# Performance work log

Measured on AMD Instinct MI355X. Metric: run time of the kernel, lower is better.

The kernel has to match this reference:

```python
import jax, jax.numpy as jnp
import numpy as np

B = 8192
D = 128
N_CLASSES = 100
TEMPERATURE = 0.1


def setup_inputs() -> dict:
    key = jax.random.key(0)
    k1, k2 = jax.random.split(key)
    feats = jax.random.normal(k1, (B, D), dtype=jnp.float32)
    # L2-normalise as the docstring assumes
    feats = feats / jnp.linalg.norm(feats, axis=1, keepdims=True)
    labels = jax.random.randint(k2, (B,), 0, N_CLASSES, dtype=jnp.int64)
    return {"features": feats, "labels": labels}


def reference(features, labels):
    features = features.astype(jnp.float32)
    b = features.shape[0]
    sim = (features @ features.T) / TEMPERATURE            # (B, B)
    labels_eq = labels[None, :] == labels[:, None]          # (B, B)
    self_mask = ~jnp.eye(b, dtype=bool)                     # (B, B), False on diag
    pos_mask = labels_eq & self_mask

    sim_max = jax.lax.stop_gradient(jnp.max(sim, axis=1, keepdims=True))
    logits = sim - sim_max                                  # (B, B)
    exp_logits = jnp.exp(logits) * self_mask.astype(jnp.float32)
    log_sum_exp = jnp.log(jnp.sum(exp_logits, axis=1, keepdims=True) + 1e-12)
    log_prob = logits - log_sum_exp                         # (B, B)

    n_positives = jnp.sum(pos_mask.astype(jnp.float32), axis=1)  # (B,)
    valid = n_positives > 0
    mean_log_prob = jnp.sum(pos_mask.astype(jnp.float32) * log_prob, axis=1) \
        / jnp.maximum(n_positives, 1.0)

    valid_f = valid.astype(jnp.float32)
    n_valid = jnp.sum(valid_f)
    loss = -jnp.sum(mean_log_prob * valid_f) / jnp.maximum(n_valid, 1.0)
    # match torch: return 0 if no anchor has a positive
    return jnp.where(n_valid > 0, loss, jnp.float32(0.0))
```

## Files before the change

kernel.cpp:

```cpp
#include <hip/hip_runtime.h>
#include <hip/hip_bf16.h>


#define BB 8192
#define DD 128
#define NCLS 100
#define NC 16
#define COLCHUNK (BB / NC)
#define NT (COLCHUNK / 16)
#define TEMP_INV 10.0f
#define MSHIFT 10.5f
#define C1F 14.426950408889634f
#define C2F -15.148297929334116f

typedef __bf16 bf16x8 __attribute__((ext_vector_type(8)));
typedef float floatx4 __attribute__((ext_vector_type(4)));

__device__ inline float fast_exp2(float x) {
#if __has_builtin(__builtin_amdgcn_exp2f)
    return __builtin_amdgcn_exp2f(x);
#else
    return exp2f(x);
#endif
}

__device__ inline unsigned short f2bf(float f) {
    unsigned u = __float_as_uint(f);
    return (unsigned short)((u + 0x7FFFu + ((u >> 16) & 1u)) >> 16);
}

__global__ __launch_bounds__(256) void supcon_convert(
    const void* __restrict__ fin, const void* __restrict__ lin,
    unsigned short* __restrict__ frag, int* __restrict__ lab,
    float* __restrict__ accbuf)
{
    int lane = threadIdx.x & 63;
    unsigned ue = ((unsigned)((const unsigned short*)fin)[2 * lane]) << 16;
    float fe = __uint_as_float(ue);
    float ve = fe * fe;
    int odd_or = ((const int*)lin)[2 * lane + 1];
#pragma unroll
    for (int m = 1; m < 64; m <<= 1) {
        ve += __shfl_xor(ve, m, 64);
        odd_or |= __shfl_xor(odd_or, m, 64);
    }
    bool f_bf16 = (ve > 0.05f) && (ve < 4.0f);
    bool l_i64  = (odd_or == 0);

    int G = blockIdx.x * 256 + threadIdx.x;
    int T = G >> 8;
    int g = (G >> 6) & 3;
    int l = G & 63;
    int col = T * 16 + (l & 15);
    int kb  = g * 32 + ((l >> 4) << 3);

    ushort4 o0, o1;
    if (!f_bf16) {
        const float4* src = (const float4*)((const float*)fin + (size_t)col * DD + kb);
        float4 a = src[0], b = src[1];
        o0.x = f2bf(a.x); o0.y = f2bf(a.y); o0.z = f2bf(a.z); o0.w = f2bf(a.w);
        o1.x = f2bf(b.x); o1.y = f2bf(b.y); o1.z = f2bf(b.z); o1.w = f2bf(b.w);
    } else {
        const ushort4* src = (const ushort4*)((const unsigned short*)fin + (size_t)col * DD + kb);
        o0 = src[0]; o1 = src[1];
    }
    ushort4* dst = (ushort4*)(frag + (size_t)G * 8);
    dst[0] = o0; dst[1] = o1;

    const int* L = (const int*)lin;
    if (blockIdx.x < 32) {
        int li = blockIdx.x * 256 + threadIdx.x;
        lab[li] = l_i64 ? L[2 * li] : L[li];
    }
    if (blockIdx.x == 0 && threadIdx.x == 0) {
        accbuf[0] = 0.0f;
        accbuf[1] = 0.0f;
        ((unsigned*)accbuf)[2] = 0u;
    }
}

#define LOADT(bb, lc, t)                                                      \
    {                                                                         \
        const unsigned char* fb =                                             \
            Fbc + ((size_t)((ctile0 + (t)) * 4) << 10) + lane * 16;           \
        _Pragma("unroll")                                                     \
        for (int k = 0; k < 4; ++k)                                           \
            bb[k] = *(const bf16x8*)(fb + (k << 10));                         \
        lc = lab[colchunkbase + (t) * 16 + l16];                              \
    }

#define COMPT(bb, lc, t)                                                      \
    {                                                                         \
        int colbase = colchunkbase + (t) * 16;                                \
        floatx4 acc[4];                                                       \
        _Pragma("unroll")                                                     \
        for (int ti = 0; ti < 4; ++ti) acc[ti] = (floatx4){0.f,0.f,0.f,0.f};  \
        _Pragma("unroll")                                                     \
        for (int k = 0; k < 4; ++k) {                                         \
            _Pragma("unroll")                                                 \
            for (int ti = 0; ti < 4; ++ti)                                    \
                acc[ti] = __builtin_amdgcn_mfma_f32_16x16x32_bf16(            \
                    afrag[ti][k], bb[k], acc[ti], 0, 0, 0);                   \
        }                                                                     \
          \
        {                                                                     \
            unsigned u = (unsigned)(colbase - (rowbase + wid * 64));          \
            if (u < 64u) {                                                    \
                _Pragma("unroll")                                             \
                for (int ti2 = 0; ti2 < 4; ++ti2) {                           \
                    if (u == (unsigned)(ti2 * 16)) {                          \
                        _Pragma("unroll")                                     \
                        for (int r = 0; r < 4; ++r)                           \
                            if (l16 == quad * 4 + r)                          \
                                diag[colbase + l16] = acc[ti2][r];            \
                    }                                                         \
                }                                                             \
            }                                                                 \
        }                                                                     \
        _Pragma("unroll")                                                     \
        for (int ti = 0; ti < 4; ++ti) {                                      \
            _Pragma("unroll")                                                 \
            for (int r = 0; r < 4; ++r) {                                     \
                        \
                int i = ti * 4 + r;                                           \
                float a = acc[ti][r];                                         \
                e_acc[i] += fast_exp2(__builtin_fmaf(a, C1F, C2F));           \
                float peq = ((lc) == lab_row[i]) ? 1.0f : 0.0f;               \
                p_acc[i] = __builtin_fmaf(peq, a, p_acc[i]);                  \
            }                                                                 \
        }                                                                     \
    }

__global__ __launch_bounds__(256, 2) void supcon_main(
    const unsigned short* __restrict__ Fb, const int* __restrict__ lab,
    float* __restrict__ e_part, float* __restrict__ p_part,
    float* __restrict__ diag)
{
    const int tid  = threadIdx.x;
    const int lane = tid & 63;
    const int wid  = tid >> 6;
    const int quad = lane >> 4;
    const int l16  = lane & 15;

    const int chunk   = blockIdx.x;
    const int rowbase = blockIdx.y * 256;
    const int colchunkbase = chunk * COLCHUNK;
    const int ctile0  = colchunkbase >> 4;

    const unsigned char* Fbc = (const unsigned char*)Fb;

    bf16x8 afrag[4][4];
#pragma unroll
    for (int ti = 0; ti < 4; ++ti) {
        int rt = (rowbase >> 4) + wid * 4 + ti;
        const unsigned char* fa = Fbc + ((size_t)(rt * 4) << 10) + lane * 16;
#pragma unroll
        for (int k = 0; k < 4; ++k)
            afrag[ti][k] = *(const bf16x8*)(fa + (k << 10));
    }

    int lab_row[16];
#pragma unroll
    for (int ti = 0; ti < 4; ++ti)
#pragma unroll
        for (int r = 0; r < 4; ++r)
            lab_row[ti * 4 + r] = lab[rowbase + wid * 64 + ti * 16 + quad * 4 + r];

    float e_acc[16], p_acc[16];
#pragma unroll
    for (int i = 0; i < 16; ++i) { e_acc[i] = 0.0f; p_acc[i] = 0.0f; }

    bf16x8 b0[4], b1[4];
    int lc0, lc1;
    LOADT(b0, lc0, 0);

    for (int t = 0; t < NT; t += 2) {
        LOADT(b1, lc1, t + 1);
        COMPT(b0, lc0, t);
        if (t + 2 < NT) LOADT(b0, lc0, t + 2);
        COMPT(b1, lc1, t + 1);
    }

#pragma unroll
    for (int i = 0; i < 16; ++i) {
        float e = e_acc[i], p = p_acc[i];
#pragma unroll
        for (int m = 1; m < 16; m <<= 1) {
            e += __shfl_xor(e, m, 64);
            p += __shfl_xor(p, m, 64);
        }
        if (l16 == 0) {
            int row = rowbase + wid * 64 + (i >> 2) * 16 + quad * 4 + (i & 3);
            e_part[(size_t)chunk * BB + row] = e;
            p_part[(size_t)chunk * BB + row] = p;
        }
    }
}

__global__ __launch_bounds__(256) void supcon_reduce(
    const float* __restrict__ e_part, const float* __restrict__ p_part,
    const int* __restrict__ labels, const float* __restrict__ diag,
    float* __restrict__ accbuf, float* __restrict__ out)
{
    __shared__ int cnt[128];
    if (threadIdx.x < 128) cnt[threadIdx.x] = 0;
    __syncthreads();
    for (int i = threadIdx.x; i < BB; i += 256)
        atomicAdd(&cnt[labels[i]], 1);
    __syncthreads();

    int row = blockIdx.x * 256 + threadIdx.x;
    float e = 0.f, p = 0.f;
#pragma unroll
    for (int c = 0; c < NC; ++c) {
        size_t idx = (size_t)c * BB + row;
        e += e_part[idx]; p += p_part[idx];
    }
    float d = diag[row];
    e -= fast_exp2(__builtin_fmaf(d, C1F, C2F));
    p -= d;
    int n_i = cnt[labels[row]] - 1;

    float contrib = 0.f, vld = 0.f;
    if (n_i > 0) {
        vld = 1.0f;
        contrib = -(p * TEMP_INV / (float)n_i - MSHIFT - logf(e));
    }
#pragma unroll
    for (int m = 1; m < 64; m <<= 1) {
        contrib += __shfl_xor(contrib, m, 64);
        vld     += __shfl_xor(vld, m, 64);
    }
    __shared__ float rl[4], rv[4];
    int lane = threadIdx.x & 63, w = threadIdx.x >> 6;
    if (lane == 0) { rl[w] = contrib; rv[w] = vld; }
    __syncthreads();
    if (threadIdx.x == 0) {
        float L = rl[0] + rl[1] + rl[2] + rl[3];
        float V = rv[0] + rv[1] + rv[2] + rv[3];
        atomicAdd(&accbuf[0], L);
        atomicAdd(&accbuf[1], V);
        __threadfence();
        unsigned t = atomicAdd((unsigned*)accbuf + 2, 1u);
        if (t == 31u) {
            float Ls = atomicAdd(&accbuf[0], 0.0f);
            float Vs = atomicAdd(&accbuf[1], 0.0f);
            out[0] = (Vs > 0.5f) ? (Ls / Vs) : 0.0f;
        }
    }
}

extern "C" void kernel_launch(void* const* d_in, const int* in_sizes, int n_in,
                              void* d_out, int out_size, void* d_ws, size_t ws_size,
                              hipStream_t stream)
{
    const void* Fin = d_in[0];
    const void* Lin = d_in[1];

    unsigned short* frag = (unsigned short*)d_ws;
    int*   lab      = (int*)((char*)d_ws + (size_t)BB * DD * 2);
    float* e_part   = (float*)((char*)lab + (size_t)BB * 4);
    float* p_part   = e_part + (size_t)NC * BB;
    float* diag     = p_part + (size_t)NC * BB;
    float* accbuf   = diag + BB;

    supcon_convert<<<BB * DD / 8 / 256, 256, 0, stream>>>(Fin, Lin, frag, lab, accbuf);

    dim3 grid(NC, BB / 256);
    supcon_main<<<grid, 256, 0, stream>>>(frag, lab, e_part, p_part, diag);

    supcon_reduce<<<32, 256, 0, stream>>>(e_part, p_part, lab, diag, accbuf, (float*)d_out);
}
```

Before: 93.88 us.

## Exploit symmetry of similarity matrix by computing only upper-triangle block pairs

Result: slower. 219.9 us (+134.2%).

```diff
diff --git a/kernel.cpp b/kernel.cpp
--- a/kernel.cpp
+++ b/kernel.cpp
@@ -5,9 +5,9 @@
 #define BB 8192
 #define DD 128
 #define NCLS 100
-#define NC 16
-#define COLCHUNK (BB / NC)
-#define NT (COLCHUNK / 16)
+#define NCH 32
+#define NC2 64
+#define NT 8
 #define TEMP_INV 10.0f
 #define MSHIFT 10.5f
 #define C1F 14.426950408889634f
@@ -86,12 +86,12 @@
         _Pragma("unroll")                                                     \
         for (int k = 0; k < 4; ++k)                                           \
             bb[k] = *(const bf16x8*)(fb + (k << 10));                         \
-        lc = lab[colchunkbase + (t) * 16 + l16];                              \
+        lc = lab[colbase0 + (t) * 16 + l16];                                  \
     }
 
 #define COMPT(bb, lc, t)                                                      \
     {                                                                         \
-        int colbase = colchunkbase + (t) * 16;                                \
+        int colbase = colbase0 + (t) * 16;                                    \
         floatx4 acc[4];                                                       \
         _Pragma("unroll")                                                     \
         for (int ti = 0; ti < 4; ++ti) acc[ti] = (floatx4){0.f,0.f,0.f,0.f};  \
@@ -102,7 +102,7 @@
                 acc[ti] = __builtin_amdgcn_mfma_f32_16x16x32_bf16(            \
                     afrag[ti][k], bb[k], acc[ti], 0, 0, 0);                   \
         }                                                                     \
-          \
+           \
         {                                                                     \
             unsigned u = (unsigned)(colbase - (rowbase + wid * 64));          \
             if (u < 64u) {                                                    \
@@ -117,6 +117,7 @@
                 }                                                             \
             }                                                                 \
         }                                                                     \
+        float cE = 0.0f, cP = 0.0f;                                           \
         _Pragma("unroll")                                                     \
         for (int ti = 0; ti < 4; ++ti) {                                      \
             _Pragma("unroll")                                                 \
@@ -124,9 +125,21 @@
                         \
                 int i = ti * 4 + r;                                           \
                 float a = acc[ti][r];                                         \
-                e_acc[i] += fast_exp2(__builtin_fmaf(a, C1F, C2F));           \
+                float ex = fast_exp2(__builtin_fmaf(a, C1F, C2F));            \
+                e_acc[i] += ex;                                               \
                 float peq = ((lc) == lab_row[i]) ? 1.0f : 0.0f;               \
                 p_acc[i] = __builtin_fmaf(peq, a, p_acc[i]);                  \
+                cE += ex;                                                     \
+                cP = __builtin_fmaf(peq, a, cP);                              \
+            }                                                                 \
+        }                                                                     \
+        if (!isdiag) {                                                        \
+                              \
+            cE += __shfl_xor(cE, 16, 64); cE += __shfl_xor(cE, 32, 64);       \
+            cP += __shfl_xor(cP, 16, 64); cP += __shfl_xor(cP, 32, 64);       \
+            if (quad == 0) {                                                  \
+                ldsE[wid][(t) * 16 + l16] = cE;      \
+                ldsP[wid][(t) * 16 + l16] = cP;                               \
             }                                                                 \
         }                                                                     \
     }
@@ -136,16 +149,28 @@
     float* __restrict__ e_part, float* __restrict__ p_part,
     float* __restrict__ diag)
 {
+    __shared__ float ldsE[4][128], ldsP[4][128];
+
     const int tid  = threadIdx.x;
     const int lane = tid & 63;
     const int wid  = tid >> 6;
     const int quad = lane >> 4;
     const int l16  = lane & 15;
 
-    const int chunk   = blockIdx.x;
-    const int rowbase = blockIdx.y * 256;
-    const int colchunkbase = chunk * COLCHUNK;
-    const int ctile0  = colchunkbase >> 4;
+    int pairIdx = blockIdx.x >> 1;
+    int h       = blockIdx.x & 1;
+    int bi = 0;
+    {
+        unsigned k = (unsigned)pairIdx;
+        while (k >= (unsigned)(NCH - bi)) { k -= (NCH - bi); ++bi; }
+        pairIdx = (int)k;
+    }
+    const int bj = bi + pairIdx;
+    const bool isdiag = (bi == bj);
+
+    const int rowbase  = bi * 256;
+    const int colbase0 = bj * 256 + h * 128;
+    const int ctile0   = colbase0 >> 4;
 
     const unsigned char* Fbc = (const unsigned char*)Fb;
 
@@ -191,8 +216,22 @@
         }
         if (l16 == 0) {
             int row = rowbase + wid * 64 + (i >> 2) * 16 + quad * 4 + (i & 3);
-            e_part[(size_t)chunk * BB + row] = e;
-            p_part[(size_t)chunk * BB + row] = p;
+            size_t base = (size_t)(2 * bj + h) * BB + row;
+            e_part[base] = e;
+            p_part[base] = p;
+        }
+    }
+
+    if (!isdiag) {
+        __syncthreads();
+        if (tid < 128) {
+            float e = ldsE[0][tid] + ldsE[1][tid] + ldsE[2][tid] + ldsE[3][tid];
+            float p = ldsP[0][tid] + ldsP[1][tid] + ldsP[2][tid] + ldsP[3][tid];
+            int j = colbase0 + tid;
+            e_part[(size_t)(2 * bi) * BB + j] = e;
+            p_part[(size_t)(2 * bi) * BB + j] = p;
+            e_part[(size_t)(2 * bi + 1) * BB + j] = 0.0f;
+            p_part[(size_t)(2 * bi + 1) * BB + j] = 0.0f;
         }
     }
 }
@@ -211,8 +250,8 @@
 
     int row = blockIdx.x * 256 + threadIdx.x;
     float e = 0.f, p = 0.f;
-#pragma unroll
-    for (int c = 0; c < NC; ++c) {
+#pragma unroll 8
+    for (int c = 0; c < NC2; ++c) {
         size_t idx = (size_t)c * BB + row;
         e += e_part[idx]; p += p_part[idx];
     }
@@ -260,14 +299,14 @@
     unsigned short* frag = (unsigned short*)d_ws;
     int*   lab      = (int*)((char*)d_ws + (size_t)BB * DD * 2);
     float* e_part   = (float*)((char*)lab + (size_t)BB * 4);
-    float* p_part   = e_part + (size_t)NC * BB;
-    float* diag     = p_part + (size_t)NC * BB;
+    float* p_part   = e_part + (size_t)NC2 * BB;
+    float* diag     = p_part + (size_t)NC2 * BB;
     float* accbuf   = diag + BB;
 
     supcon_convert<<<BB * DD / 8 / 256, 256, 0, stream>>>(Fin, Lin, frag, lab, accbuf);
 
-    dim3 grid(NC, BB / 256);
-    supcon_main<<<grid, 256, 0, stream>>>(frag, lab, e_part, p_part, diag);
+    supcon_main<<<(NCH * (NCH + 1) / 2) * 2, 256, 0, stream>>>(
+        frag, lab, e_part, p_part, diag);
 
     supcon_reduce<<<32, 256, 0, stream>>>(e_part, p_part, lab, diag, accbuf, (float*)d_out);
 }
```
